# Optimization experiments

Hardware: AMD Instinct MI355X
Metric: run time of the kernel (lower is better)

The kernel has to match this reference:

```python
import jax, jax.numpy as jnp
import numpy as np

NUM_HEADS = 16
ROPE_BASE = 10000.0


def _rotate_half(x):
    x1, x2 = jnp.split(x, 2, axis=-1)
    return jnp.concatenate([-x2, x1], axis=-1)


def _rope_cos_sin(seq_len, dim, dtype):
    # GPT-NeoX rotary: inv_freq over even dims, emb = concat(freqs, freqs)
    inv_freq = 1.0 / (ROPE_BASE ** (jnp.arange(0, dim, 2, dtype=jnp.float32) / dim))
    t = jnp.arange(seq_len, dtype=jnp.float32)
    freqs = jnp.einsum('s,d->sd', t, inv_freq)          # [S, dim/2]
    emb = jnp.concatenate([freqs, freqs], axis=-1)       # [S, dim]
    cos = jnp.cos(emb).astype(dtype)[:, None, None, :]   # [S,1,1,dim]
    sin = jnp.sin(emb).astype(dtype)[:, None, None, :]
    return cos, sin


def setup_inputs() -> dict:
    key = jax.random.key(0)
    k1, k2, k3 = jax.random.split(key, 3)
    S, B, H = 2048, 2, 2048
    x = jax.random.normal(k1, (S, B, H), dtype=jnp.float32)
    w_qkv = jax.random.normal(k2, (H, 3 * H), dtype=jnp.float32) * 0.02
    w_dense = jax.random.normal(k3, (H, H), dtype=jnp.float32) * 0.02
    return {"x": x, "w_qkv": w_qkv, "w_dense": w_dense}


def reference(x, w_qkv, w_dense):
    # x: [S, B, H] (Megatron seq-first layout)
    S, B, H = x.shape
    hd = H // NUM_HEADS

    qkv = jnp.einsum('sbh,hk->sbk', x, w_qkv)                  # fused QKV proj
    qkv = qkv.reshape(S, B, NUM_HEADS, 3 * hd)
    q, k, v = jnp.split(qkv, 3, axis=-1)                       # each [S,B,nh,hd]

    cos, sin = _rope_cos_sin(S, hd, x.dtype)
    q = q * cos + _rotate_half(q) * sin
    k = k * cos + _rotate_half(k) * sin

    norm_factor = jnp.asarray(np.sqrt(hd), dtype=x.dtype)
    scores = jnp.einsum('sbhd,tbhd->bhst', q, k) / norm_factor  # [B,nh,S,S]

    # causal mask (attention_mask_func fills masked with large negative)
    causal = jnp.tril(jnp.ones((S, S), dtype=bool))
    scores = jnp.where(causal, scores, jnp.asarray(-1e4, dtype=scores.dtype))

    # softmax in fp32 (attention_softmax_in_fp32)
    probs = jax.nn.softmax(scores.astype(jnp.float32), axis=-1).astype(x.dtype)

    ctx = jnp.einsum('bhst,tbhd->sbhd', probs, v).reshape(S, B, H)
    out = jnp.einsum('sbh,hk->sbk', ctx, w_dense)               # row-parallel dense (skip_bias_add)
    return out
```

## Files before the change

kernel.cpp:

```cpp
#include <hip/hip_runtime.h>
#include <cstdint>
#include <cstddef>

typedef _Float16 v8h __attribute__((ext_vector_type(8)));
typedef _Float16 v4h __attribute__((ext_vector_type(4)));
typedef _Float16 v2h __attribute__((ext_vector_type(2)));
typedef float v4f __attribute__((ext_vector_type(4)));
typedef float v16f __attribute__((ext_vector_type(16)));

#define NH 16
#define HD 128
#define SLEN 2048
#define BATCH 2
#define HID 2048

__device__ __forceinline__ void gload16(const void* gptr, void* lptr) {
  __builtin_amdgcn_global_load_lds(
      (const __attribute__((address_space(1))) unsigned int*)gptr,
      (__attribute__((address_space(3))) unsigned int*)lptr, 16, 0, 0);
}

__device__ __forceinline__ uint32_t pkh(float a, float b) {
  return __builtin_bit_cast(uint32_t, __builtin_amdgcn_cvt_pkrtz(a, b));
}
__device__ __forceinline__ v2h pkh2(float a, float b) {
  return __builtin_bit_cast(v2h, __builtin_amdgcn_cvt_pkrtz(a, b));
}
__device__ __forceinline__ uint32_t xswap32(uint32_t x) {
  return (uint32_t)__shfl_xor((int)x, 32, 64);
}


__global__ __launch_bounds__(256) void cast_x_kernel(const float* __restrict__ in,
                                                     _Float16* __restrict__ out, int n4) {
  int i = blockIdx.x * 256 + threadIdx.x;
  if (i >= n4) return;
  const float4 v = ((const float4*)in)[i];
  v4h o; o[0] = (_Float16)v.x; o[1] = (_Float16)v.y; o[2] = (_Float16)v.z; o[3] = (_Float16)v.w;
  *(v4h*)(out + (size_t)i * 4) = o;
}

__global__ __launch_bounds__(256) void transpose_cast_kernel(const float* __restrict__ W,
                                                             _Float16* __restrict__ WT,
                                                             int R, int C) {
  __shared__ float tl[32][33];
  int tx = threadIdx.x, ty = threadIdx.y;
  int c0 = blockIdx.x * 32, r0 = blockIdx.y * 32;
#pragma unroll
  for (int i = 0; i < 4; ++i)
    tl[ty + i * 8][tx] = W[(size_t)(r0 + ty + i * 8) * C + c0 + tx];
  __syncthreads();
#pragma unroll
  for (int i = 0; i < 4; ++i)
    WT[(size_t)(c0 + ty + i * 8) * R + r0 + tx] = (_Float16)tl[tx][ty + i * 8];
}

__global__ __launch_bounds__(256) void transpose_v_kernel(const _Float16* __restrict__ V,
                                                          _Float16* __restrict__ VT) {
  __shared__ _Float16 tl[32][33];
  int tx = threadIdx.x, ty = threadIdx.y;
  int s0 = blockIdx.x * 32, d0 = blockIdx.y * 32;
  int bh = blockIdx.z;
  const _Float16* Vp = V + (size_t)bh * SLEN * HD;
  _Float16* Tp = VT + (size_t)bh * HD * SLEN;
#pragma unroll
  for (int i = 0; i < 4; ++i)
    tl[ty + i * 8][tx] = Vp[(size_t)(s0 + ty + i * 8) * HD + d0 + tx];
  __syncthreads();
#pragma unroll
  for (int i = 0; i < 4; ++i)
    Tp[(size_t)(d0 + ty + i * 8) * SLEN + s0 + tx] = tl[tx][ty + i * 8];
}

__global__ void rope_table_kernel(float* __restrict__ cost, float* __restrict__ sint) {
  int s = blockIdx.x, i = threadIdx.x;
  float inv = powf(10000.0f, -(float)i * (1.0f / 64.0f));
  float ang = (float)s * inv;
  cost[s * 64 + i] = cosf(ang);
  sint[s * 64 + i] = sinf(ang);
}

__global__ __launch_bounds__(256) void rope_apply_kernel(_Float16* __restrict__ Q,
                                                         _Float16* __restrict__ K,
                                                         const float* __restrict__ cost,
                                                         const float* __restrict__ sint) {
  int idx = blockIdx.x * 256 + threadIdx.x;
  int dg = (idx & 7) * 8;
  int s = (idx >> 3) & (SLEN - 1);
  int bh = idx >> 14;
  size_t base = ((size_t)bh * SLEN + s) * HD;
  float4 c0 = *(const float4*)(cost + s * 64 + dg);
  float4 c1 = *(const float4*)(cost + s * 64 + dg + 4);
  float4 s0 = *(const float4*)(sint + s * 64 + dg);
  float4 s1 = *(const float4*)(sint + s * 64 + dg + 4);
  float cc[8] = {c0.x, c0.y, c0.z, c0.w, c1.x, c1.y, c1.z, c1.w};
  float ss[8] = {s0.x, s0.y, s0.z, s0.w, s1.x, s1.y, s1.z, s1.w};
  {
    v8h qa = *(const v8h*)(Q + base + dg);
    v8h qb = *(const v8h*)(Q + base + dg + 64);
#pragma unroll
    for (int j = 0; j < 8; ++j) {
      float a = (float)qa[j], b = (float)qb[j];
      qa[j] = (_Float16)(a * cc[j] - b * ss[j]);
      qb[j] = (_Float16)(b * cc[j] + a * ss[j]);
    }
    *(v8h*)(Q + base + dg) = qa;
    *(v8h*)(Q + base + dg + 64) = qb;
  }
  {
    v8h ka = *(const v8h*)(K + base + dg);
    v8h kb = *(const v8h*)(K + base + dg + 64);
#pragma unroll
    for (int j = 0; j < 8; ++j) {
      float a = (float)ka[j], b = (float)kb[j];
      ka[j] = (_Float16)(a * cc[j] - b * ss[j]);
      kb[j] = (_Float16)(b * cc[j] + a * ss[j]);
    }
    *(v8h*)(K + base + dg) = ka;
    *(v8h*)(K + base + dg + 64) = kb;
  }
}

template <int MODE>
__global__ __launch_bounds__(256) void gemm_kernel(const _Float16* __restrict__ A,
                                                   const _Float16* __restrict__ BT,
                                                   int M, int N, int K, int gy,
                                                   _Float16* __restrict__ q_out,
                                                   _Float16* __restrict__ k_out,
                                                   _Float16* __restrict__ v_out,
                                                   float* __restrict__ f_out) {
  __shared__ alignas(16) char As[2][16384];
  __shared__ alignas(16) char Bs[2][16384];
  const int t = threadIdx.x;
  const int w = t >> 6;
  const int l = t & 63;
  const int wr = w >> 1, wc = w & 1;

  const int total = gridDim.x;
  const int F = blockIdx.x;
  const int gid = (F & 7) * (total >> 3) + (F >> 3);
  const int bx = gid / gy, by = gid % gy;
  const int m0 = by * 128;
  const int n0 = bx * 128;

  const char* aS[4];
  const char* bS[4];
  {
    const int Kb = K * 2;
#pragma unroll
    for (int j = 0; j < 4; ++j) {
      int c = w * 256 + j * 64 + l;
      int row = c >> 3;
      int col = ((c & 7) * 16) ^ ((row & 7) << 4);
      aS[j] = (const char*)A + (size_t)(m0 + row) * Kb + col;
      bS[j] = (const char*)BT + (size_t)(n0 + row) * Kb + col;
    }
  }

  const v4f vzero = {0.f, 0.f, 0.f, 0.f};
  v4f acc[4][4];
#pragma unroll
  for (int mi = 0; mi < 4; ++mi)
#pragma unroll
    for (int ni = 0; ni < 4; ++ni) acc[mi][ni] = vzero;

  auto stage = [&](int ks, int d) {
#pragma unroll
    for (int j = 0; j < 4; ++j) {
      gload16(aS[j] + ks * 128, &As[d][w * 4096 + j * 1024]);
      gload16(bS[j] + ks * 128, &Bs[d][w * 4096 + j * 1024]);
    }
  };

  const int nk = K >> 6;
  stage(0, 0);
  for (int ks = 0; ks < nk; ++ks) {
    asm volatile("s_waitcnt vmcnt(0)" ::: "memory");
    __syncthreads();
    if (ks + 1 < nk) stage(ks + 1, (ks + 1) & 1);
    const char* Ap = As[ks & 1];
    const char* Bp = Bs[ks & 1];
#pragma unroll
    for (int kk = 0; kk < 2; ++kk) {
      v8h a[4], b[4];
#pragma unroll
      for (int mi = 0; mi < 4; ++mi) {
        int row = wr * 64 + mi * 16 + (l & 15);
        a[mi] = *(const v8h*)(Ap + row * 128 + ((kk * 64 + ((l >> 4) * 16)) ^ ((row & 7) << 4)));
      }
#pragma unroll
      for (int ni = 0; ni < 4; ++ni) {
        int row = wc * 64 + ni * 16 + (l & 15);
        b[ni] = *(const v8h*)(Bp + row * 128 + ((kk * 64 + ((l >> 4) * 16)) ^ ((row & 7) << 4)));
      }
      __builtin_amdgcn_s_setprio(1);
#pragma unroll
      for (int mi = 0; mi < 4; ++mi)
#pragma unroll
        for (int ni = 0; ni < 4; ++ni)
          acc[mi][ni] = __builtin_amdgcn_mfma_f32_16x16x32_f16(a[mi], b[ni], acc[mi][ni], 0, 0, 0);
      __builtin_amdgcn_s_setprio(0);
    }
  }

#pragma unroll
  for (int mi = 0; mi < 4; ++mi) {
#pragma unroll
    for (int ni = 0; ni < 4; ++ni) {
      int n = n0 + wc * 64 + ni * 16 + (l & 15);
#pragma unroll
      for (int r = 0; r < 4; ++r) {
        int m = m0 + wr * 64 + mi * 16 + (l >> 4) * 4 + r;
        float v = acc[mi][ni][r];
        if (MODE == 1) {
          f_out[(size_t)m * N + n] = v;
        } else {
          int head = n / 384;
          int rem = n - head * 384;
          int seg = rem >> 7;
          int d = rem & 127;
          int s = m >> 1, bb = m & 1;
          _Float16* dst = (seg == 0) ? q_out : (seg == 1) ? k_out : v_out;
          dst[(((size_t)(bb * NH + head)) * SLEN + s) * HD + d] = (_Float16)v;
        }
      }
    }
  }
}

__global__ __launch_bounds__(256, 2) void attn_kernel(const _Float16* __restrict__ Qb,
                                                      const _Float16* __restrict__ Kb,
                                                      const _Float16* __restrict__ VTb,
                                                      _Float16* __restrict__ ctx) {
  __shared__ alignas(16) char Ks[2][16384];
  __shared__ alignas(16) char Vs[2][16384];
  const int t = threadIdx.x;
  const int w = t >> 6;
  const int l = t & 63;
  const int F = blockIdx.x;
  const int bh = (F & 7) + 8 * ((F >> 3) & 3);
  const int pr = F >> 5;
  const int ta = pr, tb = 31 - pr;
  const int grp = w >> 1;
  const int tile = grp ? tb : ta;
  const int q0 = tile * 64 + (w & 1) * 32;
  const int l31 = l & 31, g = l >> 5;
  const int q = q0 + l31;

  const _Float16* Qp = Qb + (size_t)bh * SLEN * HD;
  const _Float16* Kp = Kb + (size_t)bh * SLEN * HD;
  const _Float16* Vp = VTb + (size_t)bh * HD * SLEN;

  const char* kS[4];
  const char* vS[4];
#pragma unroll
  for (int j = 0; j < 4; ++j) {
    int c = w * 256 + j * 64 + l;
    {
      int row = c >> 4;
      int col = ((c & 15) * 16) ^ ((row & 7) << 4);
      kS[j] = (const char*)Kp + (size_t)row * 256 + col;
    }
    {
      int row = c >> 3;
      int col = ((c & 7) * 16) ^ ((row & 7) << 4);
      vS[j] = (const char*)Vp + (size_t)row * (SLEN * 2) + col;
    }
  }
  auto stage = [&](int kt, int d) {
#pragma unroll
    for (int j = 0; j < 4; ++j) {
      gload16(kS[j] + (size_t)kt * 16384, &Ks[d][w * 4096 + j * 1024]);
      gload16(vS[j] + (size_t)kt * 128, &Vs[d][w * 4096 + j * 1024]);
    }
  };

  v8h qf[8];
#pragma unroll
  for (int c = 0; c < 8; ++c)
    qf[c] = *(const v8h*)(Qp + (size_t)q * HD + c * 16 + g * 8);

  v16f oT[4];
#pragma unroll
  for (int dc = 0; dc < 4; ++dc)
#pragma unroll
    for (int r = 0; r < 16; ++r) oT[dc][r] = 0.f;
  float m_run = -1e30f, l_run = 0.f;
  const float scale = 0.08838834764831845f;

  stage(0, 0);
  for (int kt = 0; kt <= tb; ++kt) {
    asm volatile("s_waitcnt vmcnt(0)" ::: "memory");
    __syncthreads();
    if (kt < tb) stage(kt + 1, (kt + 1) & 1);
    if (grp == 0 && kt > ta) continue;
    const char* Kst = Ks[kt & 1];
    const char* Vst = Vs[kt & 1];

    v16f s0, s1;
#pragma unroll
    for (int r = 0; r < 16; ++r) { s0[r] = 0.f; s1[r] = 0.f; }
    __builtin_amdgcn_s_setprio(1);
#pragma unroll
    for (int c = 0; c < 8; ++c) {
      int cofs = (c * 32 + g * 16);
      v8h kf0 = *(const v8h*)(Kst + l31 * 256 + (cofs ^ ((l31 & 7) << 4)));
      v8h kf1 = *(const v8h*)(Kst + (32 + l31) * 256 + (cofs ^ ((l31 & 7) << 4)));
      s0 = __builtin_amdgcn_mfma_f32_32x32x16_f16(kf0, qf[c], s0, 0, 0, 0);
      s1 = __builtin_amdgcn_mfma_f32_32x32x16_f16(kf1, qf[c], s1, 0, 0, 0);
    }
    __builtin_amdgcn_s_setprio(0);

    const bool diag = (kt == tile);
    const int kv0 = kt * 64;
    float pv[32];
#pragma unroll
    for (int r = 0; r < 16; ++r) {
      int kofs = (r & 3) + 8 * (r >> 2) + 4 * g;
      float a = s0[r] * scale;
      float b = s1[r] * scale;
      if (diag) {
        if (kv0 + kofs > q) a = -1e4f;
        if (kv0 + 32 + kofs > q) b = -1e4f;
      }
      pv[r] = a;
      pv[16 + r] = b;
    }

    float mx[8];
#pragma unroll
    for (int i = 0; i < 8; ++i)
      mx[i] = fmaxf(fmaxf(pv[i], pv[i + 8]), fmaxf(pv[i + 16], pv[i + 24]));
    float pm = fmaxf(fmaxf(fmaxf(mx[0], mx[1]), fmaxf(mx[2], mx[3])),
                     fmaxf(fmaxf(mx[4], mx[5]), fmaxf(mx[6], mx[7])));
    float pmall = fmaxf(pm, __shfl_xor(pm, 32, 64));

    float mnew;
    if (__all(pmall - m_run <= 8.f)) {
      mnew = m_run;
    } else {
      mnew = fmaxf(m_run, pmall);
      float alpha = __expf(m_run - mnew);
      m_run = mnew;
      l_run *= alpha;
#pragma unroll
      for (int dc = 0; dc < 4; ++dc)
#pragma unroll
        for (int r = 0; r < 16; ++r) oT[dc][r] *= alpha;
    }

    float sacc0 = 0.f, sacc1 = 0.f, sacc2 = 0.f, sacc3 = 0.f;
#pragma unroll
    for (int i = 0; i < 8; ++i) { pv[i] = __expf(pv[i] - mnew); sacc0 += pv[i]; }
#pragma unroll
    for (int i = 8; i < 16; ++i) { pv[i] = __expf(pv[i] - mnew); sacc1 += pv[i]; }
#pragma unroll
    for (int i = 16; i < 24; ++i) { pv[i] = __expf(pv[i] - mnew); sacc2 += pv[i]; }
#pragma unroll
    for (int i = 24; i < 32; ++i) { pv[i] = __expf(pv[i] - mnew); sacc3 += pv[i]; }
    float ssum = (sacc0 + sacc1) + (sacc2 + sacc3);
    l_run += ssum + __shfl_xor(ssum, 32, 64);

    __builtin_amdgcn_s_setprio(1);
#pragma unroll
    for (int c = 0; c < 4; ++c) {
      int base = (c >> 1) * 16 + (c & 1) * 8;
      uint32_t P0 = pkh(pv[base + 0], pv[base + 1]);
      uint32_t P1 = pkh(pv[base + 2], pv[base + 3]);
      uint32_t P2 = pkh(pv[base + 4], pv[base + 5]);
      uint32_t P3 = pkh(pv[base + 6], pv[base + 7]);
      uint32_t T0 = g ? P0 : P2;
      uint32_t T1 = g ? P1 : P3;
      uint32_t U0 = xswap32(T0);
      uint32_t U1 = xswap32(T1);
      union { uint32_t u[4]; v8h h; } pu;
      pu.u[0] = g ? U0 : P0;
      pu.u[1] = g ? U1 : P1;
      pu.u[2] = g ? P2 : U0;
      pu.u[3] = g ? P3 : U1;
      v8h pf = pu.h;
      int cofs = c * 32 + g * 16;
#pragma unroll
      for (int dc = 0; dc < 4; ++dc) {
        int vrow = dc * 32 + l31;
        v8h vf = *(const v8h*)(Vst + vrow * 128 + (cofs ^ ((vrow & 7) << 4)));
        oT[dc] = __builtin_amdgcn_mfma_f32_32x32x16_f16(vf, pf, oT[dc], 0, 0, 0);
      }
    }
    __builtin_amdgcn_s_setprio(0);
  }

  const float inv = 1.0f / l_run;
  const int b = bh >> 4;
  const int hh = bh & 15;
  _Float16* orow = ctx + ((size_t)q * BATCH + b) * HID + hh * HD;
#pragma unroll
  for (int dc = 0; dc < 4; ++dc) {
#pragma unroll
    for (int rr = 0; rr < 4; ++rr) {
      v2h w0 = pkh2(oT[dc][4 * rr + 0] * inv, oT[dc][4 * rr + 1] * inv);
      v2h w1 = pkh2(oT[dc][4 * rr + 2] * inv, oT[dc][4 * rr + 3] * inv);
      v4h o4; o4[0] = w0[0]; o4[1] = w0[1]; o4[2] = w1[0]; o4[3] = w1[1];
      *(v4h*)(orow + dc * 32 + rr * 8 + g * 4) = o4;
    }
  }
}


extern "C" void kernel_launch(void* const* d_in, const int* in_sizes, int n_in,
                              void* d_out, int out_size, void* d_ws, size_t ws_size,
                              hipStream_t stream) {
  const float* x = (const float*)d_in[0];
  const float* w_qkv = (const float*)d_in[1];
  const float* w_dense = (const float*)d_in[2];
  float* out = (float*)d_out;
  char* ws = (char*)d_ws;

  _Float16* xb    = (_Float16*)(ws);
  _Float16* wqkvT = (_Float16*)(ws + 16777216);
  _Float16* wdT   = (_Float16*)(ws + 41943040);
  _Float16* Qb    = (_Float16*)(ws + 50331648);
  _Float16* Kb    = (_Float16*)(ws + 67108864);
  _Float16* Vb    = (_Float16*)(ws + 83886080);
  _Float16* VTb   = (_Float16*)(ws + 100663296);
  _Float16* ctx   = (_Float16*)(ws + 117440512);
  float* cost     = (float*)(ws + 134217728);
  float* sint     = (float*)(ws + 134742016);

  cast_x_kernel<<<dim3(8192), dim3(256), 0, stream>>>(x, xb, 2097152);
  transpose_cast_kernel<<<dim3(192, 64), dim3(32, 8), 0, stream>>>(w_qkv, wqkvT, 2048, 6144);
  transpose_cast_kernel<<<dim3(64, 64), dim3(32, 8), 0, stream>>>(w_dense, wdT, 2048, 2048);
  rope_table_kernel<<<dim3(2048), dim3(64), 0, stream>>>(cost, sint);

  gemm_kernel<0><<<dim3(1536), dim3(256), 0, stream>>>(xb, wqkvT, 4096, 6144, 2048, 32,
                                                       Qb, Kb, Vb, (float*)nullptr);
  rope_apply_kernel<<<dim3(2048), dim3(256), 0, stream>>>(Qb, Kb, cost, sint);
  transpose_v_kernel<<<dim3(64, 4, 32), dim3(32, 8), 0, stream>>>(Vb, VTb);
  attn_kernel<<<dim3(512), dim3(256), 0, stream>>>(Qb, Kb, VTb, ctx);
  gemm_kernel<1><<<dim3(512), dim3(256), 0, stream>>>(ctx, wdT, 4096, 2048, 2048, 32,
                                                      (_Float16*)nullptr, (_Float16*)nullptr,
                                                      (_Float16*)nullptr, out);
}
```

Before: 284.1 us.

## Use 256x256-tile 512-thread GEMM kernel for fused QKV projection

Adds a new GEMM kernel with 256x256 output tiles, 8 waves per block, and 64 KB of double-buffered LDS per operand pair. The QKV projection launches it with 384 blocks instead of 1536 blocks of the smaller-tile kernel. The aim is more operand reuse per LDS load and less global traffic per FLOP. In exchange it uses more registers and LDS, allowing only one block per CU, and 384 blocks over 256 CUs leaves the last wave partly empty.

```diff
diff --git a/kernel.cpp b/kernel.cpp
--- a/kernel.cpp
+++ b/kernel.cpp
@@ -122,6 +122,127 @@
 }
 
 template <int MODE>
+__global__ __launch_bounds__(512, 1) void gemm256_kernel(const _Float16* __restrict__ A,
+                                                         const _Float16* __restrict__ BT,
+                                                         int M, int N, int K, int gy,
+                                                         _Float16* __restrict__ q_out,
+                                                         _Float16* __restrict__ k_out,
+                                                         _Float16* __restrict__ v_out,
+                                                         float* __restrict__ f_out) {
+  __shared__ alignas(16) char As[2][32768];
+  __shared__ alignas(16) char Bs[2][32768];
+  const int t = threadIdx.x;
+  const int w = t >> 6;
+  const int l = t & 63;
+  const int wr = w >> 2, wc = w & 3;
+
+  const int total = gridDim.x;
+  const int F = blockIdx.x;
+  const int gid = (F & 7) * (total >> 3) + (F >> 3);
+  const int bx = gid / gy, by = gid % gy;
+  const int m0 = by * 256;
+  const int n0 = bx * 256;
+
+  const char* aS[4];
+  const char* bS[4];
+  {
+    const int Kb = K * 2;
+#pragma unroll
+    for (int j = 0; j < 4; ++j) {
+      int c = w * 256 + j * 64 + l;
+      int row = c >> 3;
+      int col = ((c & 7) * 16) ^ ((row & 7) << 4);
+      aS[j] = (const char*)A + (size_t)(m0 + row) * Kb + col;
+      bS[j] = (const char*)BT + (size_t)(n0 + row) * Kb + col;
+    }
+  }
+
+  const v4f vzero = {0.f, 0.f, 0.f, 0.f};
+  v4f acc[8][4];
+#pragma unroll
+  for (int mi = 0; mi < 8; ++mi)
+#pragma unroll
+    for (int ni = 0; ni < 4; ++ni) acc[mi][ni] = vzero;
+
+  auto stage = [&](int ks, int d) {
+#pragma unroll
+    for (int j = 0; j < 4; ++j) {
+      gload16(aS[j] + ks * 128, &As[d][w * 4096 + j * 1024]);
+      gload16(bS[j] + ks * 128, &Bs[d][w * 4096 + j * 1024]);
+    }
+  };
+
+  const int nk = K >> 6;
+  stage(0, 0);
+  for (int ks = 0; ks < nk; ++ks) {
+    asm volatile("s_waitcnt vmcnt(0)" ::: "memory");
+    __syncthreads();
+    if (ks + 1 < nk) stage(ks + 1, (ks + 1) & 1);
+    const char* Ap = As[ks & 1];
+    const char* Bp = Bs[ks & 1];
+
+    v8h b[4][2];
+#pragma unroll
+    for (int ni = 0; ni < 4; ++ni) {
+      int row = wc * 64 + ni * 16 + (l & 15);
+#pragma unroll
+      for (int kk = 0; kk < 2; ++kk)
+        b[ni][kk] = *(const v8h*)(Bp + row * 128 +
+                                  ((kk * 64 + ((l >> 4) * 16)) ^ ((row & 7) << 4)));
+    }
+
+#pragma unroll
+    for (int p = 0; p < 4; ++p) {
+      v8h a[2][2];
+#pragma unroll
+      for (int i2 = 0; i2 < 2; ++i2) {
+        int row = wr * 128 + (2 * p + i2) * 16 + (l & 15);
+#pragma unroll
+        for (int kk = 0; kk < 2; ++kk)
+          a[i2][kk] = *(const v8h*)(Ap + row * 128 +
+                                    ((kk * 64 + ((l >> 4) * 16)) ^ ((row & 7) << 4)));
+      }
+      __builtin_amdgcn_s_setprio(1);
+#pragma unroll
+      for (int i2 = 0; i2 < 2; ++i2)
+#pragma unroll
+        for (int ni = 0; ni < 4; ++ni)
+#pragma unroll
+          for (int kk = 0; kk < 2; ++kk)
+            acc[2 * p + i2][ni] =
+                __builtin_amdgcn_mfma_f32_16x16x32_f16(a[i2][kk], b[ni][kk],
+                                                       acc[2 * p + i2][ni], 0, 0, 0);
+      __builtin_amdgcn_s_setprio(0);
+      if (p < 3) __syncthreads();
+    }
+  }
+
+#pragma unroll
+  for (int mi = 0; mi < 8; ++mi) {
+#pragma unroll
+    for (int ni = 0; ni < 4; ++ni) {
+      int n = n0 + wc * 64 + ni * 16 + (l & 15);
+#pragma unroll
+      for (int r = 0; r < 4; ++r) {
+        int m = m0 + wr * 128 + mi * 16 + (l >> 4) * 4 + r;
+        float v = acc[mi][ni][r];
+        if (MODE == 1) {
+          f_out[(size_t)m * N + n] = v;
+        } else {
+          int head = n / 384;
+          int rem = n - head * 384;
+          int seg = rem >> 7;
+          int d = rem & 127;
+          int s = m >> 1, bb = m & 1;
+          _Float16* dst = (seg == 0) ? q_out : (seg == 1) ? k_out : v_out;
+          dst[(((size_t)(bb * NH + head)) * SLEN + s) * HD + d] = (_Float16)v;
+        }
+      }
+    }
+  }
+}
+
+template <int MODE>
 __global__ __launch_bounds__(256) void gemm_kernel(const _Float16* __restrict__ A,
                                                    const _Float16* __restrict__ BT,
                                                    int M, int N, int K, int gy,
@@ -432,8 +553,8 @@
   transpose_cast_kernel<<<dim3(64, 64), dim3(32, 8), 0, stream>>>(w_dense, wdT, 2048, 2048);
   rope_table_kernel<<<dim3(2048), dim3(64), 0, stream>>>(cost, sint);
 
-  gemm_kernel<0><<<dim3(1536), dim3(256), 0, stream>>>(xb, wqkvT, 4096, 6144, 2048, 32,
-                                                       Qb, Kb, Vb, (float*)nullptr);
+  gemm256_kernel<0><<<dim3(384), dim3(512), 0, stream>>>(xb, wqkvT, 4096, 6144, 2048, 16,
+                                                         Qb, Kb, Vb, (float*)nullptr);
   rope_apply_kernel<<<dim3(2048), dim3(256), 0, stream>>>(Qb, Kb, cost, sint);
   transpose_v_kernel<<<dim3(64, 4, 32), dim3(32, 8), 0, stream>>>(Vb, VTb);
   attn_kernel<<<dim3(512), dim3(256), 0, stream>>>(Qb, Kb, VTb, ctx);
```

Measured after the change: 305.0 us. 7.4% more time.
